# Optimization experiments

Hardware: AMD Instinct MI355X
Metric: run time of the kernel (lower is better)

Reference implementation:

```python
import jax, jax.numpy as jnp
import numpy as np


def setup_inputs() -> dict:
    key = jax.random.key(0)
    k1, k2 = jax.random.split(key)
    IN, OUT, N = 4096, 4096, 8192
    x = jax.random.normal(k1, (N, IN), dtype=jnp.float32)
    fc = jnp.arange(OUT, dtype=jnp.float32).reshape(-1, 1)  # learned param, init = arange
    bias = jax.random.normal(k2, (OUT,), dtype=jnp.float32) * 0.5
    return {"x": x, "fc": fc, "bias": bias}


def _dst_matrix(fc, in_features, dtype):
    out_features = fc.shape[0]
    t = jnp.arange(in_features, dtype=dtype)[None, :]          # [1, in]
    # torch.eye(out, 1): column vector, 1 at row 0 else 0
    eye_col = jnp.zeros((out_features, 1), dtype=dtype).at[0, 0].set(1.0)
    norm = jax.lax.rsqrt(2.0 * in_features * (eye_col + 1.0))  # [out, 1]
    # dst_m[k, t] = 2 * norm[k] * sin(pi/2 * (k+1)/in * (2t+1))
    dst_m = 2.0 * norm * jnp.sin(0.5 * jnp.pi * ((fc + 1.0) / in_features) * (2.0 * t + 1.0))
    return dst_m  # [out, in]


def reference(x, fc, bias):
    in_features = x.shape[-1]
    w = _dst_matrix(fc, in_features, x.dtype)  # [out, in]
    # F.linear: y = x @ w.T + bias
    return jnp.einsum('ni,oi->no', x, w) + bias
```

## Files before the change

kernel.cpp:

```cpp
#include <hip/hip_runtime.h>
#include <cstdint>
#include <cstddef>

#define IN_F 4096
#define OUT_F 4096
#define NROWS 8192
#define PI_F 3.14159265358979323846f

#define PD(a) ((a) + ((a) >> 4))

__device__ inline float2 cmul(float2 a, float2 b) {
    return make_float2(a.x * b.x - a.y * b.y, a.x * b.y + a.y * b.x);
}

__global__ void twprep(float2* __restrict__ tw, float2* __restrict__ f3,
                       float2* __restrict__ f23) {
    const int i = blockIdx.x * 256 + threadIdx.x;
    float s, c;
    if (i < 1024) {
        sincosf(-PI_F * (float)i / 1024.0f, &s, &c);
        tw[i] = make_float2(c, s);
    }
    sincosf(-PI_F * (float)i / 8192.0f, &s, &c);
    f3[i] = make_float2(c, s);
    sincosf(-PI_F * 5.0f * (float)i / 8192.0f, &s, &c);
    f23[i] = make_float2(c, s);
}

struct c4 { float2 z0, z1, z2, z3; };
__device__ __forceinline__ c4 r4unit(float2 x0, float2 x1, float2 x2, float2 x3) {
    const float2 E = make_float2(x0.x + x2.x, x0.y + x2.y);
    const float2 G = make_float2(x0.x - x2.x, x0.y - x2.y);
    const float2 F = make_float2(x1.x + x3.x, x1.y + x3.y);
    const float2 H = make_float2(x1.x - x3.x, x1.y - x3.y);
    c4 r;
    r.z0 = make_float2(E.x + F.x, E.y + F.y);
    r.z2 = make_float2(E.x - F.x, E.y - F.y);
    r.z1 = make_float2(G.x + H.y, G.y - H.x);
    r.z3 = make_float2(G.x - H.y, G.y + H.x);
    return r;
}

__global__ __launch_bounds__(512, 6) void dst_row(const float* __restrict__ x,
                                                  const float* __restrict__ bias,
                                                  const float2* __restrict__ twg,
                                                  const float2* __restrict__ f3,
                                                  const float2* __restrict__ f23,
                                                  float* __restrict__ out) {
    __shared__ float2 VV[2][2176];
    __shared__ float2 TW[1024];
    const int t = threadIdx.x;
    const int row0 = blockIdx.x * 2;
    const float* xr0 = x + (size_t)row0 * IN_F;
    const float* xr1 = xr0 + IN_F;
    float2* VA = VV[0];
    float2* VB = VV[1];

    {
        const float2 w1 = twg[t];
        const float2 w2 = twg[2 * t];
        const float2 w3 = cmul(w1, w2);
        {
            const float4 v0 = *(const float4*)(xr0 + 4 * t);
            const float4 v1 = *(const float4*)(xr0 + 4 * (t + 512));
            const float4 v2 = *(const float4*)(xr0 + (4092 - 4 * t));
            const float4 v3 = *(const float4*)(xr0 + (2044 - 4 * t));
            const c4 r = r4unit(make_float2(v0.x, v0.z), make_float2(v1.x, v1.z),
                                make_float2(-v2.w, -v2.y), make_float2(-v3.w, -v3.y));
            VA[PD(t)]        = r.z0;
            VA[PD(t + 512)]  = cmul(w1, r.z1);
            VA[PD(t + 1024)] = cmul(w2, r.z2);
            VA[PD(t + 1536)] = cmul(w3, r.z3);
        }
        {
            const float4 v0 = *(const float4*)(xr1 + 4 * t);
            const float4 v1 = *(const float4*)(xr1 + 4 * (t + 512));
            const float4 v2 = *(const float4*)(xr1 + (4092 - 4 * t));
            const float4 v3 = *(const float4*)(xr1 + (2044 - 4 * t));
            const c4 r = r4unit(make_float2(v0.x, v0.z), make_float2(v1.x, v1.z),
                                make_float2(-v2.w, -v2.y), make_float2(-v3.w, -v3.y));
            VB[PD(t)]        = r.z0;
            VB[PD(t + 512)]  = cmul(w1, r.z1);
            VB[PD(t + 1024)] = cmul(w2, r.z2);
            VB[PD(t + 1536)] = cmul(w3, r.z3);
        }
        TW[t] = w1;
        TW[t + 512] = twg[t + 512];
    }
    __syncthreads();

    for (int s = 1; s < 5; ++s) {
        const int h = 512 >> (2 * s);
        const int i = t & (h - 1);
        const int base = ((t >> (9 - 2 * s)) << (11 - 2 * s)) + i;
        const float2 u1 = TW[i << (2 * s)];
        const float2 u2 = TW[i << (2 * s + 1)];
        const float2 u3 = cmul(u1, u2);
        const int p0 = PD(base), p1 = PD(base + h), p2 = PD(base + 2 * h), p3 = PD(base + 3 * h);
        {
            const c4 r = r4unit(VA[p0], VA[p1], VA[p2], VA[p3]);
            VA[p0] = r.z0;
            VA[p1] = cmul(u1, r.z1);
            VA[p2] = cmul(u2, r.z2);
            VA[p3] = cmul(u3, r.z3);
        }
        {
            const c4 r = r4unit(VB[p0], VB[p1], VB[p2], VB[p3]);
            VB[p0] = r.z0;
            VB[p1] = cmul(u1, r.z1);
            VB[p2] = cmul(u2, r.z2);
            VB[p3] = cmul(u3, r.z3);
        }
        __syncthreads();
    }

    const int rr = t >> 8;
    const int u = t & 255;
    const float2* V = VV[rr];
    float* yr = out + (size_t)(row0 + rr) * OUT_F;
    const float amp1 = 2.0f * rsqrtf(8192.0f);
    const float amp0 = 2.0f * rsqrtf(16384.0f);
#pragma unroll
    for (int q = 0; q < 8; ++q) {
        const int k = u + (q << 8);
        const int P = ((k & 3) << 9) | (((k >> 2) & 3) << 7) | (((k >> 4) & 3) << 5)
                    | (((k >> 6) & 3) << 3) | (((k >> 8) & 3) << 1);
        const float2 a = V[PD(P)];
        const float2 b = V[PD(P) + 1];
        const float2 z = (k < 1024) ? make_float2(a.x + b.x, a.y + b.y)
                                    : make_float2(a.x - b.x, a.y - b.y);
        const int kc = (2048 - k) & 2047;
        const int Pc = ((kc & 3) << 9) | (((kc >> 2) & 3) << 7) | (((kc >> 4) & 3) << 5)
                     | (((kc >> 6) & 3) << 3) | (((kc >> 8) & 3) << 1);
        const float2 ac = V[PD(Pc)];
        const float2 bc = V[PD(Pc) + 1];
        const float2 zc = (kc < 1024) ? make_float2(ac.x + bc.x, ac.y + bc.y)
                                      : make_float2(ac.x - bc.x, ac.y - bc.y);
        const float Arr = 0.5f * (z.x + zc.x), Aii = 0.5f * (z.y - zc.y);
        const float Brr = 0.5f * (z.y + zc.y), Bii = 0.5f * (zc.x - z.x);
        const float2 e3 = f3[k];
        const float2 eA = f23[k];
        const float Wr = Arr * e3.x - Aii * e3.y + Brr * eA.x - Bii * eA.y;
        const float Wi = Arr * e3.y + Aii * e3.x + Brr * eA.y + Bii * eA.x;
        const int o1 = 4095 - k;
        yr[o1] = amp1 * Wr + bias[o1];
        if (k > 0) {
            const int o2 = k - 1;
            const float amp = (o2 == 0) ? amp0 : amp1;
            yr[o2] = amp * (-Wi) + bias[o2];
        } else {
            const float C2048 = (z.x - z.y) * 0.70710678118654752f;
            yr[2047] = amp1 * C2048 + bias[2047];
        }
    }
}

__global__ __launch_bounds__(256) void dst_row_fb(const float* __restrict__ x,
                                                  const float* __restrict__ bias,
                                                  float* __restrict__ out) {
    __shared__ float Ar[2048], Ai[2048], Br[2048], Bi[2048];
    const int t = threadIdx.x;
    const int row = blockIdx.x;
    const float* xr = x + (size_t)row * IN_F;
    float* yr = out + (size_t)row * OUT_F;
#pragma unroll
    for (int q = 0; q < 8; ++q) {
        const int m = t + q * 256;
        float re, im;
        if (m < 1024) {
            const float4 v = *(const float4*)(xr + 4 * m);
            re = v.x; im = v.z;
        } else {
            const float4 v = *(const float4*)(xr + (8188 - 4 * m));
            re = -v.w; im = -v.y;
        }
        Ar[m] = re; Ai[m] = im;
    }
    __syncthreads();
    float *sr = Ar, *si = Ai, *dr = Br, *di = Bi;
    for (int s = 0; s < 11; ++s) {
        const int mm = 1024 >> s;
#pragma unroll
        for (int q = 0; q < 4; ++q) {
            const int b = t + q * 256;
            const int j = b >> (10 - s);
            const int i = b & (mm - 1);
            const int i0 = i + j * 2 * mm;
            const float ar = sr[i0], aim = si[i0];
            const float cr = sr[i0 + mm], ci = si[i0 + mm];
            float sw, cw;
            __sincosf(-PI_F * (float)j / (float)(1 << s), &sw, &cw);
            const float wr = cr * cw - ci * sw;
            const float wi = cr * sw + ci * cw;
            const int o0 = i + j * mm;
            dr[o0] = ar + wr;        di[o0] = aim + wi;
            dr[o0 + 1024] = ar - wr; di[o0 + 1024] = aim - wi;
        }
        __syncthreads();
        float* tp;
        tp = sr; sr = dr; dr = tp;
        tp = si; si = di; di = tp;
    }
    const float amp1 = 2.0f * rsqrtf(8192.0f);
    const float amp0 = 2.0f * rsqrtf(16384.0f);
#pragma unroll
    for (int q = 0; q < 8; ++q) {
        const int k = t + q * 256;
        const float zr = sr[k], zi = si[k];
        const int kc = (2048 - k) & 2047;
        const float cr = sr[kc], ci = si[kc];
        const float Arr = 0.5f * (zr + cr), Aii = 0.5f * (zi - ci);
        const float Brr = 0.5f * (zi + ci), Bii = 0.5f * (cr - zr);
        float s2, c2;
        __sincosf(-PI_F * (float)k / 2048.0f, &s2, &c2);
        const float Vr = Arr + Brr * c2 - Bii * s2;
        const float Vi = Aii + Brr * s2 + Bii * c2;
        float s3, c3;
        __sincosf(-PI_F * (float)k / 8192.0f, &s3, &c3);
        const float Wr = Vr * c3 - Vi * s3;
        const float Wi = Vr * s3 + Vi * c3;
        const int o1 = 4095 - k;
        yr[o1] = amp1 * Wr + bias[o1];
        if (k > 0) {
            const int o2 = k - 1;
            const float amp = (o2 == 0) ? amp0 : amp1;
            yr[o2] = amp * (-Wi) + bias[o2];
        } else {
            const float C2048 = (zr - zi) * 0.70710678118654752f;
            yr[2047] = amp1 * C2048 + bias[2047];
        }
    }
}

extern "C" void kernel_launch(void* const* d_in, const int* in_sizes, int n_in,
                              void* d_out, int out_size, void* d_ws, size_t ws_size,
                              hipStream_t stream) {
    const float* x    = (const float*)d_in[0];
    const float* bias = (const float*)d_in[2];
    float* out = (float*)d_out;

    if (ws_size >= 40960) {
        float2* tw  = (float2*)d_ws;
        float2* f3  = (float2*)((char*)d_ws + 8192);
        float2* f23 = (float2*)((char*)d_ws + 24576);
        twprep<<<8, 256, 0, stream>>>(tw, f3, f23);
        dst_row<<<NROWS / 2, 512, 0, stream>>>(x, bias, tw, f3, f23, out);
    } else {
        dst_row_fb<<<NROWS, 256, 0, stream>>>(x, bias, out);
    }
}
```

Measured before the change: 95.91 us.

## Drop intra-wave FFT stage barriers, keep twiddles in registers, repad LDS

Unrolls the four radix-4 stages into a templated helper. Stages 3 and 4 only exchange data within a single wavefront, so the block-wide barriers before them become an LDS wait-count fence. Per-stage twiddles are now loaded from global memory into registers at kernel start, which removes the shared twiddle table, one LDS read pass per stage and one barrier. The LDS padding formula adds extra skew every 128 elements to cut bank conflicts. The costs are more live registers under the occupancy bound of 6 and a dependence on in-order LDS access within a wavefront for correctness.

```diff
diff --git a/kernel.cpp b/kernel.cpp
--- a/kernel.cpp
+++ b/kernel.cpp
@@ -7,7 +7,8 @@
 #define NROWS 8192
 #define PI_F 3.14159265358979323846f
 
-#define PD(a) ((a) + ((a) >> 4))
+#define PD(a) ((a) + ((a) >> 4) + 3 * ((a) >> 7))
+#define ROWSTR 2224
 
 __device__ inline float2 cmul(float2 a, float2 b) {
     return make_float2(a.x * b.x - a.y * b.y, a.x * b.y + a.y * b.x);
@@ -41,14 +42,34 @@
     return r;
 }
 
+template<int S>
+__device__ __forceinline__ void dif4(float2* __restrict__ V, int t,
+                                     float2 u1, float2 u2) {
+    const int h = 512 >> (2 * S);
+    const int i = t & (h - 1);
+    const int base = ((t >> (9 - 2 * S)) << (11 - 2 * S)) + i;
+    const float2 u3 = cmul(u1, u2);
+    const int p0 = PD(base), p1 = PD(base + h), p2 = PD(base + 2 * h),
+              p3 = PD(base + 3 * h);
+    const c4 r = r4unit(V[p0], V[p1], V[p2], V[p3]);
+    V[p0] = r.z0;
+    V[p1] = cmul(u1, r.z1);
+    V[p2] = cmul(u2, r.z2);
+    V[p3] = cmul(u3, r.z3);
+}
+
+#define WFENCE do { \
+    asm volatile("s_waitcnt lgkmcnt(0)" ::: "memory"); \
+    __builtin_amdgcn_sched_barrier(0); \
+} while (0)
+
 __global__ __launch_bounds__(512, 6) void dst_row(const float* __restrict__ x,
                                                   const float* __restrict__ bias,
                                                   const float2* __restrict__ twg,
                                                   const float2* __restrict__ f3,
                                                   const float2* __restrict__ f23,
                                                   float* __restrict__ out) {
-    __shared__ float2 VV[2][2176];
-    __shared__ float2 TW[1024];
+    __shared__ float2 VV[2][ROWSTR];
     const int t = threadIdx.x;
     const int row0 = blockIdx.x * 2;
     const float* xr0 = x + (size_t)row0 * IN_F;
@@ -56,9 +77,18 @@
     float2* VA = VV[0];
     float2* VB = VV[1];
 
+    const float2 w1 = twg[t];
+    const float2 w2 = twg[2 * t];
+    const float2 s1u1 = twg[(t & 127) << 2];
+    const float2 s1u2 = twg[(t & 127) << 3];
+    const float2 s2u1 = twg[(t & 31) << 4];
+    const float2 s2u2 = twg[(t & 31) << 5];
+    const float2 s3u1 = twg[(t & 7) << 6];
+    const float2 s3u2 = twg[(t & 7) << 7];
+    const float2 s4u1 = twg[(t & 1) << 8];
+    const float2 s4u2 = twg[(t & 1) << 9];
+
     {
-        const float2 w1 = twg[t];
-        const float2 w2 = twg[2 * t];
         const float2 w3 = cmul(w1, w2);
         {
             const float4 v0 = *(const float4*)(xr0 + 4 * t);
@@ -84,35 +114,22 @@
             VB[PD(t + 1024)] = cmul(w2, r.z2);
             VB[PD(t + 1536)] = cmul(w3, r.z3);
         }
-        TW[t] = w1;
-        TW[t + 512] = twg[t + 512];
-    }
-    __syncthreads();
-
-    for (int s = 1; s < 5; ++s) {
-        const int h = 512 >> (2 * s);
-        const int i = t & (h - 1);
-        const int base = ((t >> (9 - 2 * s)) << (11 - 2 * s)) + i;
-        const float2 u1 = TW[i << (2 * s)];
-        const float2 u2 = TW[i << (2 * s + 1)];
-        const float2 u3 = cmul(u1, u2);
-        const int p0 = PD(base), p1 = PD(base + h), p2 = PD(base + 2 * h), p3 = PD(base + 3 * h);
-        {
-            const c4 r = r4unit(VA[p0], VA[p1], VA[p2], VA[p3]);
-            VA[p0] = r.z0;
-            VA[p1] = cmul(u1, r.z1);
-            VA[p2] = cmul(u2, r.z2);
-            VA[p3] = cmul(u3, r.z3);
-        }
-        {
-            const c4 r = r4unit(VB[p0], VB[p1], VB[p2], VB[p3]);
-            VB[p0] = r.z0;
-            VB[p1] = cmul(u1, r.z1);
-            VB[p2] = cmul(u2, r.z2);
-            VB[p3] = cmul(u3, r.z3);
-        }
-        __syncthreads();
-    }
+    }
+    __syncthreads();
+
+    dif4<1>(VA, t, s1u1, s1u2);
+    dif4<1>(VB, t, s1u1, s1u2);
+    __syncthreads();
+
+    dif4<2>(VA, t, s2u1, s2u2);
+    dif4<2>(VB, t, s2u1, s2u2);
+    WFENCE;
+    dif4<3>(VA, t, s3u1, s3u2);
+    dif4<3>(VB, t, s3u1, s3u2);
+    WFENCE;
+    dif4<4>(VA, t, s4u1, s4u2);
+    dif4<4>(VB, t, s4u1, s4u2);
+    __syncthreads();
 
     const int rr = t >> 8;
     const int u = t & 255;
```

Result: faster. 89.65 us (-6.5%).
